# Performance work log

Measured on AMD Instinct MI355X. Metric: run time of the kernel, lower is better.

## Reference

```python
import jax, jax.numpy as jnp
import numpy as np

EPS = 1e-8
N_AGENTS = 8
N_ACTIONS = 10
STATE_NUM = 100
EMBED_DIM = 32
Q_MIN, Q_MAX = -10.0, 10.0
NOISE_COEF = 0.1
LOGDET_COEF = 1.0


def setup_inputs() -> dict:
    key = jax.random.key(0)
    k1, k2, k3, k4, k5 = jax.random.split(key, 5)
    n1, n2 = 4096, 64
    agent_qs = jax.random.normal(k1, (n1, n2, N_AGENTS), dtype=jnp.float32)
    states = jax.random.randint(k2, (n1, n2, N_AGENTS), 0, STATE_NUM)
    actions = jax.random.randint(k3, (n1, n2, N_AGENTS), 0, N_ACTIONS)
    noise = jax.random.uniform(k4, (n1 * n2, N_AGENTS), dtype=jnp.float32)
    # Embedding table: n_agents * state_num * n_actions rows, row-normalized at init
    W = jax.random.normal(k5, (N_AGENTS * STATE_NUM * N_ACTIONS, EMBED_DIM), dtype=jnp.float32)
    W = W / jnp.maximum(jnp.linalg.norm(W, axis=1, keepdims=True), 1e-12)
    return {"agent_qs": agent_qs, "states": states, "actions": actions,
            "noise": noise, "B_weight": W}


def reference(agent_qs, states, actions, noise, B_weight):
    n1, n2, nA = agent_qs.shape
    bias_base = STATE_NUM * N_ACTIONS
    state_bias = bias_base * jnp.arange(nA)  # (nA,)

    qs = jnp.clip(agent_qs, Q_MIN, Q_MAX).reshape(-1, nA)  # (bs, nA)
    idx = states.reshape(-1, nA) * N_ACTIONS + actions.reshape(-1, nA) + state_bias
    B = B_weight[idx]  # (bs, nA, E) embedding gather
    # F.normalize(p=2, dim=2)
    B = B / jnp.maximum(jnp.linalg.norm(B, axis=2, keepdims=True), 1e-12)

    # BBT + diag(noise)*coef, relu + eps, batched det/log over tiny nA x nA matrices
    BBT = jnp.einsum('bie,bje->bij', B, B)
    BBT = BBT + noise[:, :, None] * jnp.eye(nA, dtype=BBT.dtype) * NOISE_COEF
    BBT = jax.nn.relu(BBT) + EPS
    det_BBT = jnp.linalg.det(BBT)
    logdet = jnp.log(det_BBT + EPS)

    q = qs.sum(axis=-1) + LOGDET_COEF * logdet
    return q.reshape(n1, n2, 1)
```

## Files before the change

kernel.cpp:

```cpp
#include <hip/hip_runtime.h>
#include <hip/hip_fp16.h>


constexpr int   NA         = 8;
constexpr float Q_MIN      = -10.0f;
constexpr float Q_MAX      = 10.0f;
constexpr float NOISE_COEF = 0.1f;
constexpr float EPS        = 1e-8f;

typedef _Float16 half2_t __attribute__((ext_vector_type(2)));

__device__ __forceinline__ float dot2(half2_t a, half2_t b, float c) {
#if __has_builtin(__builtin_amdgcn_fdot2)
    return __builtin_amdgcn_fdot2(a, b, c, false);
#else
    return fmaf((float)a.x, (float)b.x, fmaf((float)a.y, (float)b.y, c));
#endif
}

__device__ __forceinline__ float qadd1(float x) {
    return x + __builtin_bit_cast(float,
        __builtin_amdgcn_mov_dpp(__builtin_bit_cast(int, x), 0xB1, 0xF, 0xF, true));
}
__device__ __forceinline__ float qadd2(float x) {
    return x + __builtin_bit_cast(float,
        __builtin_amdgcn_mov_dpp(__builtin_bit_cast(int, x), 0x4E, 0xF, 0xF, true));
}

__global__ __launch_bounds__(256) void convert_kernel(
    const float* __restrict__ W, __half* __restrict__ W16, int n4)
{
    int t = blockIdx.x * blockDim.x + threadIdx.x;
    if (t >= n4) return;
    float4 v = reinterpret_cast<const float4*>(W)[t];
    ushort4 h;
    h.x = __half_as_ushort(__float2half(v.x));
    h.y = __half_as_ushort(__float2half(v.y));
    h.z = __half_as_ushort(__float2half(v.z));
    h.w = __half_as_ushort(__float2half(v.w));
    reinterpret_cast<ushort4*>(W16)[t] = h;
}

__global__ __launch_bounds__(256, 4) void qdpp_kernel(
    const float* __restrict__ agent_qs,
    const int*   __restrict__ states,
    const int*   __restrict__ actions,
    const float* __restrict__ noise,
    const __half* __restrict__ W16,
    float*       __restrict__ out,
    int bs)
{
    int tid = blockIdx.x * blockDim.x + threadIdx.x;
    int e = tid >> 2;
    int l = tid & 3;
    if (e >= bs) return;
    size_t base = (size_t)e * NA;

    int4 s0 = *reinterpret_cast<const int4*>(states + base);
    int4 s1 = *reinterpret_cast<const int4*>(states + base + 4);
    int4 a0 = *reinterpret_cast<const int4*>(actions + base);
    int4 a1 = *reinterpret_cast<const int4*>(actions + base + 4);

    int lb = 8 * l;
    int off[8];
    off[0] = (s0.x * 10 + a0.x        ) * 32 + lb;
    off[1] = (s0.y * 10 + a0.y + 1000 ) * 32 + lb;
    off[2] = (s0.z * 10 + a0.z + 2000 ) * 32 + lb;
    off[3] = (s0.w * 10 + a0.w + 3000 ) * 32 + lb;
    off[4] = (s1.x * 10 + a1.x + 4000 ) * 32 + lb;
    off[5] = (s1.y * 10 + a1.y + 5000 ) * 32 + lb;
    off[6] = (s1.z * 10 + a1.z + 6000 ) * 32 + lb;
    off[7] = (s1.w * 10 + a1.w + 7000 ) * 32 + lb;

    uint4 raw[8];
    #pragma unroll
    for (int i = 0; i < 8; i++)
        raw[i] = *reinterpret_cast<const uint4*>(W16 + off[i]);

    float4 qa = *reinterpret_cast<const float4*>(agent_qs + base);
    float4 qb = *reinterpret_cast<const float4*>(agent_qs + base + 4);
    float4 n0 = *reinterpret_cast<const float4*>(noise + base);
    float4 n1 = *reinterpret_cast<const float4*>(noise + base + 4);

    half2_t h[8][4];
    #pragma unroll
    for (int i = 0; i < 8; i++) {
        h[i][0] = __builtin_bit_cast(half2_t, raw[i].x);
        h[i][1] = __builtin_bit_cast(half2_t, raw[i].y);
        h[i][2] = __builtin_bit_cast(half2_t, raw[i].z);
        h[i][3] = __builtin_bit_cast(half2_t, raw[i].w);
    }

    float g[8][8];
    #pragma unroll
    for (int i = 0; i < 8; i++) {
        #pragma unroll
        for (int j = i; j < 8; j++) {
            float acc = dot2(h[i][0], h[j][0], 0.0f);
            acc = dot2(h[i][1], h[j][1], acc);
            acc = dot2(h[i][2], h[j][2], acc);
            acc = dot2(h[i][3], h[j][3], acc);
            g[i][j] = acc;
        }
    }

    #pragma unroll
    for (int i = 0; i < 8; i++)
        #pragma unroll
        for (int j = i; j < 8; j++)
            g[i][j] = qadd2(qadd1(g[i][j]));

    float qsum = fminf(fmaxf(qa.x, Q_MIN), Q_MAX) + fminf(fmaxf(qa.y, Q_MIN), Q_MAX)
               + fminf(fmaxf(qa.z, Q_MIN), Q_MAX) + fminf(fmaxf(qa.w, Q_MIN), Q_MAX)
               + fminf(fmaxf(qb.x, Q_MIN), Q_MAX) + fminf(fmaxf(qb.y, Q_MIN), Q_MAX)
               + fminf(fmaxf(qb.z, Q_MIN), Q_MAX) + fminf(fmaxf(qb.w, Q_MIN), Q_MAX);

    float nz[8] = {n0.x, n0.y, n0.z, n0.w, n1.x, n1.y, n1.z, n1.w};

    float m[8][8];
    float pgii = 1.0f;
    #pragma unroll
    for (int i = 0; i < 8; i++) {
        pgii *= g[i][i];
        #pragma unroll
        for (int j = 0; j < 8; j++) {
            if (i == j) {
                m[i][i] = g[i][i] * fmaf(NOISE_COEF, nz[i], 1.0f + EPS);
            } else {
                float gij = (j > i) ? g[i][j] : g[j][i];
                m[i][j] = fmaxf(gij, 0.0f);
            }
        }
    }

    float det = 1.0f;
    #pragma unroll
    for (int k = 0; k < 8; k++) {
        float p = m[k][k];
        det *= p;
        float ip = __builtin_amdgcn_rcpf(p);
        #pragma unroll
        for (int i = k + 1; i < 8; i++) {
            float f = m[i][k] * ip;
            #pragma unroll
            for (int j = k + 1; j < 8; j++)
                m[i][j] = fmaf(-f, m[k][j], m[i][j]);
        }
    }

    float detM = det * __builtin_amdgcn_rcpf(pgii);
    if (l == 0)
        out[e] = qsum + __logf(detM + EPS);
}

extern "C" void kernel_launch(void* const* d_in, const int* in_sizes, int n_in,
                              void* d_out, int out_size, void* d_ws, size_t ws_size,
                              hipStream_t stream) {
    const float* agent_qs = (const float*)d_in[0];
    const int*   states   = (const int*)d_in[1];
    const int*   actions  = (const int*)d_in[2];
    const float* noise    = (const float*)d_in[3];
    const float* W        = (const float*)d_in[4];
    float*       out      = (float*)d_out;
    __half*      W16      = (__half*)d_ws;

    int wn = in_sizes[4];
    int n4 = wn / 4;
    convert_kernel<<<(n4 + 255) / 256, 256, 0, stream>>>(W, W16, n4);

    int bs = in_sizes[0] / NA;
    const int block = 256;
    long long total = (long long)bs * 4;
    int grid = (int)((total + block - 1) / block);
    qdpp_kernel<<<grid, block, 0, stream>>>(agent_qs, states, actions, noise, W16, out, bs);
}
```

Measured before the change: 96.43 us.

## Compute Gram matrices with MFMA 16x16x32 and redistribute through LDS

Replaces the per-thread fdot2 Gram computation and DPP cross-lane reductions with one MFMA f16 16x16x32 per pair of elements: each wave packs two elements' eight embeddings into a 16x32 tile and multiplies it by its own transpose. The 16x16 result is staged in shared memory, and each element's 8x8 block is read back by lanes that then run the existing elimination. This moves the dot-product arithmetic onto matrix cores and removes shuffle reductions. It adds LDS traffic and a block barrier, and it computes redundant off-diagonal blocks. The launch grid is unchanged, and the code assumes the batch size divides evenly, since the bounds check was removed.

```diff
diff --git a/kernel.cpp b/kernel.cpp
--- a/kernel.cpp
+++ b/kernel.cpp
@@ -8,24 +8,8 @@
 constexpr float NOISE_COEF = 0.1f;
 constexpr float EPS        = 1e-8f;
 
-typedef _Float16 half2_t __attribute__((ext_vector_type(2)));
-
-__device__ __forceinline__ float dot2(half2_t a, half2_t b, float c) {
-#if __has_builtin(__builtin_amdgcn_fdot2)
-    return __builtin_amdgcn_fdot2(a, b, c, false);
-#else
-    return fmaf((float)a.x, (float)b.x, fmaf((float)a.y, (float)b.y, c));
-#endif
-}
-
-__device__ __forceinline__ float qadd1(float x) {
-    return x + __builtin_bit_cast(float,
-        __builtin_amdgcn_mov_dpp(__builtin_bit_cast(int, x), 0xB1, 0xF, 0xF, true));
-}
-__device__ __forceinline__ float qadd2(float x) {
-    return x + __builtin_bit_cast(float,
-        __builtin_amdgcn_mov_dpp(__builtin_bit_cast(int, x), 0x4E, 0xF, 0xF, true));
-}
+typedef _Float16 f16x8 __attribute__((ext_vector_type(8)));
+typedef float    f32x4 __attribute__((ext_vector_type(4)));
 
 __global__ __launch_bounds__(256) void convert_kernel(
     const float* __restrict__ W, __half* __restrict__ W16, int n4)
@@ -50,88 +34,69 @@
     float*       __restrict__ out,
     int bs)
 {
-    int tid = blockIdx.x * blockDim.x + threadIdx.x;
-    int e = tid >> 2;
-    int l = tid & 3;
-    if (e >= bs) return;
-    size_t base = (size_t)e * NA;
+    __shared__ __align__(16) float lds[4 * 8 * 260];
 
-    int4 s0 = *reinterpret_cast<const int4*>(states + base);
-    int4 s1 = *reinterpret_cast<const int4*>(states + base + 4);
-    int4 a0 = *reinterpret_cast<const int4*>(actions + base);
-    int4 a1 = *reinterpret_cast<const int4*>(actions + base + 4);
+    int lane = threadIdx.x & 63;
+    int wave = threadIdx.x >> 6;
+    int e_base = (blockIdx.x * 4 + wave) * 16;
 
-    int lb = 8 * l;
-    int off[8];
-    off[0] = (s0.x * 10 + a0.x        ) * 32 + lb;
-    off[1] = (s0.y * 10 + a0.y + 1000 ) * 32 + lb;
-    off[2] = (s0.z * 10 + a0.z + 2000 ) * 32 + lb;
-    off[3] = (s0.w * 10 + a0.w + 3000 ) * 32 + lb;
-    off[4] = (s1.x * 10 + a1.x + 4000 ) * 32 + lb;
-    off[5] = (s1.y * 10 + a1.y + 5000 ) * 32 + lb;
-    off[6] = (s1.z * 10 + a1.z + 6000 ) * 32 + lb;
-    off[7] = (s1.w * 10 + a1.w + 7000 ) * 32 + lb;
+    int a  = lane & 7;
+    int b8 = (lane >> 3) & 1;
+    int c4 = lane >> 4;
 
     uint4 raw[8];
     #pragma unroll
-    for (int i = 0; i < 8; i++)
-        raw[i] = *reinterpret_cast<const uint4*>(W16 + off[i]);
+    for (int p = 0; p < 8; p++) {
+        int ep = e_base + 2 * p + b8;
+        int s  = states [ep * NA + a];
+        int ac = actions[ep * NA + a];
+        int off = (s * 10 + ac + 1000 * a) * 32 + 8 * c4;
+        raw[p] = *reinterpret_cast<const uint4*>(W16 + off);
+    }
+
+    float* ldsw = lds + wave * 2080;
+    int wr = (lane & 15) * 16 + (lane >> 4) * 4;
+    #pragma unroll
+    for (int p = 0; p < 8; p++) {
+        f32x4 acc = {0.0f, 0.0f, 0.0f, 0.0f};
+        f16x8 f = __builtin_bit_cast(f16x8, raw[p]);
+        acc = __builtin_amdgcn_mfma_f32_16x16x32_f16(f, f, acc, 0, 0, 0);
+        *reinterpret_cast<f32x4*>(ldsw + p * 260 + wr) = acc;
+    }
+
+    __syncthreads();
+
+    int q  = lane >> 2;
+    int e  = e_base + q;
+    size_t base = (size_t)e * NA;
+    int pq = q >> 1, bq = q & 1;
+    const float* rb = ldsw + pq * 260 + 136 * bq;
 
     float4 qa = *reinterpret_cast<const float4*>(agent_qs + base);
     float4 qb = *reinterpret_cast<const float4*>(agent_qs + base + 4);
     float4 n0 = *reinterpret_cast<const float4*>(noise + base);
     float4 n1 = *reinterpret_cast<const float4*>(noise + base + 4);
+    float nz[8] = {n0.x, n0.y, n0.z, n0.w, n1.x, n1.y, n1.z, n1.w};
 
-    half2_t h[8][4];
+    float m[8][8];
+    float pgii = 1.0f;
     #pragma unroll
-    for (int i = 0; i < 8; i++) {
-        h[i][0] = __builtin_bit_cast(half2_t, raw[i].x);
-        h[i][1] = __builtin_bit_cast(half2_t, raw[i].y);
-        h[i][2] = __builtin_bit_cast(half2_t, raw[i].z);
-        h[i][3] = __builtin_bit_cast(half2_t, raw[i].w);
+    for (int j = 0; j < 8; j++) {
+        float4 lo = *reinterpret_cast<const float4*>(rb + j * 16);
+        float4 hi = *reinterpret_cast<const float4*>(rb + j * 16 + 4);
+        float v[8] = {lo.x, lo.y, lo.z, lo.w, hi.x, hi.y, hi.z, hi.w};
+        #pragma unroll
+        for (int i = 0; i < 8; i++)
+            m[i][j] = fmaxf(v[i], 0.0f);
+        float gjj = v[j];
+        pgii *= gjj;
+        m[j][j] = gjj * fmaf(NOISE_COEF, nz[j], 1.0f + EPS);
     }
-
-    float g[8][8];
-    #pragma unroll
-    for (int i = 0; i < 8; i++) {
-        #pragma unroll
-        for (int j = i; j < 8; j++) {
-            float acc = dot2(h[i][0], h[j][0], 0.0f);
-            acc = dot2(h[i][1], h[j][1], acc);
-            acc = dot2(h[i][2], h[j][2], acc);
-            acc = dot2(h[i][3], h[j][3], acc);
-            g[i][j] = acc;
-        }
-    }
-
-    #pragma unroll
-    for (int i = 0; i < 8; i++)
-        #pragma unroll
-        for (int j = i; j < 8; j++)
-            g[i][j] = qadd2(qadd1(g[i][j]));
 
     float qsum = fminf(fmaxf(qa.x, Q_MIN), Q_MAX) + fminf(fmaxf(qa.y, Q_MIN), Q_MAX)
                + fminf(fmaxf(qa.z, Q_MIN), Q_MAX) + fminf(fmaxf(qa.w, Q_MIN), Q_MAX)
                + fminf(fmaxf(qb.x, Q_MIN), Q_MAX) + fminf(fmaxf(qb.y, Q_MIN), Q_MAX)
                + fminf(fmaxf(qb.z, Q_MIN), Q_MAX) + fminf(fmaxf(qb.w, Q_MIN), Q_MAX);
-
-    float nz[8] = {n0.x, n0.y, n0.z, n0.w, n1.x, n1.y, n1.z, n1.w};
-
-    float m[8][8];
-    float pgii = 1.0f;
-    #pragma unroll
-    for (int i = 0; i < 8; i++) {
-        pgii *= g[i][i];
-        #pragma unroll
-        for (int j = 0; j < 8; j++) {
-            if (i == j) {
-                m[i][i] = g[i][i] * fmaf(NOISE_COEF, nz[i], 1.0f + EPS);
-            } else {
-                float gij = (j > i) ? g[i][j] : g[j][i];
-                m[i][j] = fmaxf(gij, 0.0f);
-            }
-        }
-    }
 
     float det = 1.0f;
     #pragma unroll
@@ -149,7 +114,7 @@
     }
 
     float detM = det * __builtin_amdgcn_rcpf(pgii);
-    if (l == 0)
+    if ((lane & 3) == 0)
         out[e] = qsum + __logf(detM + EPS);
 }
 
```

New measurement: 96.37 us. Within noise of the previous version (-0.1%).
